# Performance work log

Measured on AMD Instinct MI355X. Metric: run time of the kernel, lower is better.

The kernel has to match this reference:

```python
import jax, jax.numpy as jnp
import numpy as np

N_NODES = 100000
N_EDGES = 1600000
N_FEATS = 64
HID1 = 128
HID2 = 128


def setup_inputs() -> dict:
    key = jax.random.key(0)
    ks = jax.random.split(key, 8)
    x = jax.random.normal(ks[0], (N_NODES, N_FEATS), dtype=jnp.float32)
    edge_index = jax.random.randint(ks[1], (2, N_EDGES), 0, N_NODES, dtype=jnp.int64)
    # glorot-ish init for linear weights (out_feats, in_feats), bias zeros (PyG default)
    W1 = jax.random.normal(ks[2], (HID1, N_FEATS), dtype=jnp.float32) * (1.0 / np.sqrt(N_FEATS))
    b1 = jnp.zeros((HID1,), dtype=jnp.float32)
    W2 = jax.random.normal(ks[3], (HID2, HID1), dtype=jnp.float32) * (1.0 / np.sqrt(HID1))
    b2 = jnp.zeros((HID2,), dtype=jnp.float32)
    W3 = jax.random.normal(ks[4], (N_FEATS, HID2), dtype=jnp.float32) * (1.0 / np.sqrt(HID2))
    b3 = jnp.zeros((N_FEATS,), dtype=jnp.float32)
    return {"x": x, "edge_index": edge_index, "W1": W1, "b1": b1,
            "W2": W2, "b2": b2, "W3": W3, "b3": b3}


def _gcn_conv(x, src, dst, norm, W, b, n_nodes):
    # dense linear transform first (out_dim may differ from in_dim)
    h = x @ W.T                                   # [N, out]
    msg = h[src] * norm[:, None]                  # gather + edge-normalize, [E+N, out]
    out = jax.ops.segment_sum(msg, dst, num_segments=n_nodes)  # scatter-add
    return out + b


def reference(x, edge_index, W1, b1, W2, b2, W3, b3):
    n = x.shape[0]
    loop = jnp.arange(n, dtype=edge_index.dtype)
    src = jnp.concatenate([edge_index[0], loop])  # self-loops appended (PyG default)
    dst = jnp.concatenate([edge_index[1], loop])
    # symmetric normalization: deg over target column incl. self-loops
    deg = jax.ops.segment_sum(jnp.ones(dst.shape, dtype=x.dtype), dst, num_segments=n)
    dinv = jnp.where(deg > 0, jax.lax.rsqrt(deg), 0.0)
    norm = dinv[src] * dinv[dst]                  # [E+N]

    h = jax.nn.relu(_gcn_conv(x, src, dst, norm, W1, b1, n))
    h = jax.nn.relu(_gcn_conv(h, src, dst, norm, W2, b2, n))
    h = _gcn_conv(h, src, dst, norm, W3, b3, n)
    return jax.nn.softmax(h, axis=1)
```

## Files before the change

kernel.cpp:

```cpp
#include <hip/hip_runtime.h>
#include <hip/hip_bf16.h>


#define NB1 256

typedef __attribute__((ext_vector_type(4))) _Float16 half4;
typedef __attribute__((ext_vector_type(8))) _Float16 half8;


__global__ __launch_bounds__(256) void k_hist(const int* __restrict__ dst, int E, int C,
                                              int NBUK, int* __restrict__ gh) {
  __shared__ int h[512];
  int t = threadIdx.x, b = blockIdx.x;
  for (int i = t; i < NBUK; i += 256) h[i] = 0;
  __syncthreads();
  int beg = b * C, end = min(beg + C, E);
  for (int i = beg + t; i < end; i += 256) atomicAdd(&h[dst[i] >> 8], 1);
  __syncthreads();
  for (int i = t; i < NBUK; i += 256) gh[i * NB1 + b] = h[i];
}

__global__ __launch_bounds__(256) void k_sum256(const int* __restrict__ g, int L,
                                                int* __restrict__ part) {
  __shared__ int red[256];
  int t = threadIdx.x;
  int idx = blockIdx.x * 256 + t;
  red[t] = (idx < L) ? g[idx] : 0;
  __syncthreads();
  for (int off = 128; off > 0; off >>= 1) {
    if (t < off) red[t] += red[t + off];
    __syncthreads();
  }
  if (t == 0) part[blockIdx.x] = red[0];
}

__global__ __launch_bounds__(512) void k_scan_part(int* __restrict__ part, int NP) {
  __shared__ int sh[512];
  int t = threadIdx.x;
  int v = (t < NP) ? part[t] : 0;
  sh[t] = v;
  __syncthreads();
  for (int off = 1; off < 512; off <<= 1) {
    int u = (t >= off) ? sh[t - off] : 0;
    __syncthreads();
    sh[t] += u;
    __syncthreads();
  }
  if (t < NP) part[t] = sh[t] - v;
}

__global__ __launch_bounds__(256) void k_scan_apply(const int* __restrict__ g, int L,
                                                    const int* __restrict__ part,
                                                    int* __restrict__ gout) {
  __shared__ int sh[256];
  int t = threadIdx.x;
  int idx = blockIdx.x * 256 + t;
  int v = (idx < L) ? g[idx] : 0;
  sh[t] = v;
  __syncthreads();
  for (int off = 1; off < 256; off <<= 1) {
    int u = (t >= off) ? sh[t - off] : 0;
    __syncthreads();
    sh[t] += u;
    __syncthreads();
  }
  if (idx < L) gout[idx] = part[blockIdx.x] + sh[t] - v;
}

__global__ __launch_bounds__(256) void k_scatter(const int* __restrict__ src,
                                                 const int* __restrict__ dst, int E, int C,
                                                 int NBUK, const int* __restrict__ gscan,
                                                 int* __restrict__ epak) {
  __shared__ int cur[512];
  int t = threadIdx.x, b = blockIdx.x;
  for (int i = t; i < NBUK; i += 256) cur[i] = gscan[i * NB1 + b];
  __syncthreads();
  int beg = b * C, end = min(beg + C, E);
  for (int i = beg + t; i < end; i += 256) {
    int d = dst[i];
    int p = atomicAdd(&cur[d >> 8], 1);
    epak[p] = src[i] | ((d & 255) << 24);
  }
}

__global__ __launch_bounds__(256) void k_csr(const int* __restrict__ epak,
                                             const int* __restrict__ gscan, int NBUK, int N, int E,
                                             int* __restrict__ rowptr, float* __restrict__ dinv,
                                             int* __restrict__ col) {
  __shared__ int cnt[256];
  __shared__ int scn[256];
  __shared__ int cur[256];
  int b = blockIdx.x, t = threadIdx.x;
  int ebeg = gscan[b * NB1];
  int eend = (b + 1 < NBUK) ? gscan[(b + 1) * NB1] : E;
  cnt[t] = 0;
  __syncthreads();
  for (int i = ebeg + t; i < eend; i += 256) atomicAdd(&cnt[(epak[i] >> 24) & 255], 1);
  __syncthreads();
  int c = cnt[t];
  scn[t] = c;
  __syncthreads();
  for (int off = 1; off < 256; off <<= 1) {
    int v = (t >= off) ? scn[t - off] : 0;
    __syncthreads();
    scn[t] += v;
    __syncthreads();
  }
  int excl = scn[t] - c;
  int node = b * 256 + t;
  if (node < N) {
    rowptr[node] = ebeg + excl;
    dinv[node] = rsqrtf((float)(c + 1));
  }
  cur[t] = ebeg + excl;
  __syncthreads();
  for (int i = ebeg + t; i < eend; i += 256) {
    int e = epak[i];
    int p = atomicAdd(&cur[(e >> 24) & 255], 1);
    col[p] = e & 0xFFFFFF;
  }
  if (b == 0 && t == 0) rowptr[N] = E;
}

__global__ __launch_bounds__(256) void k_prescaleh(const float* __restrict__ x,
                                                   const float* __restrict__ dinv,
                                                   _Float16* __restrict__ xp, int N) {
  int i = blockIdx.x * 256 + threadIdx.x;
  if (i < N * 16) {
    int row = i >> 4;
    float4 v = ((const float4*)x)[i];
    float d = dinv[row];
    half4 o;
    o[0] = (_Float16)(v.x * d);
    o[1] = (_Float16)(v.y * d);
    o[2] = (_Float16)(v.z * d);
    o[3] = (_Float16)(v.w * d);
    ((half4*)xp)[i] = o;
  }
}


template <int EPI>
__global__ __launch_bounds__(256) void k_agg64h(const _Float16* __restrict__ hp,
                                                const float* __restrict__ dinv,
                                                const int* __restrict__ rowptr,
                                                const int* __restrict__ col,
                                                const float* __restrict__ bias,
                                                float* __restrict__ out, int N) {
  int wid = blockIdx.x * 4 + (threadIdx.x >> 6);
  int lane = threadIdx.x & 63;
  if (wid >= N) return;
  int g = lane >> 3;
  int fl = (lane & 7) * 8;
  float acc[8] = {0.f, 0.f, 0.f, 0.f, 0.f, 0.f, 0.f, 0.f};
  int r0 = rowptr[wid], r1 = rowptr[wid + 1];
  for (int base = r0; base < r1; base += 64) {
    int mm = min(64, r1 - base);
    int ce = (base + lane < r1) ? col[base + lane] : 0;
    for (int j = 0; j < mm; j += 16) {
      int i0 = j + g, i1 = j + 8 + g;
      int s0 = __shfl(ce, i0);
      int s1 = __shfl(ce, i1);
      if (i0 < mm) {
        half8 v = *(const half8*)&hp[(size_t)s0 * 64 + fl];
#pragma unroll
        for (int k = 0; k < 8; ++k) acc[k] += (float)v[k];
      }
      if (i1 < mm) {
        half8 v = *(const half8*)&hp[(size_t)s1 * 64 + fl];
#pragma unroll
        for (int k = 0; k < 8; ++k) acc[k] += (float)v[k];
      }
    }
  }
#pragma unroll
  for (int o = 8; o < 64; o <<= 1) {
#pragma unroll
    for (int k = 0; k < 8; ++k) acc[k] += __shfl_xor(acc[k], o);
  }
  half8 sv = *(const half8*)&hp[(size_t)wid * 64 + fl];
  float di = dinv[wid];
  float v[8];
#pragma unroll
  for (int k = 0; k < 8; ++k) v[k] = di * (acc[k] + (float)sv[k]);
  if (EPI == 1) {
    float4 ba = *(const float4*)&bias[fl];
    float4 bb = *(const float4*)&bias[fl + 4];
    v[0] += ba.x; v[1] += ba.y; v[2] += ba.z; v[3] += ba.w;
    v[4] += bb.x; v[5] += bb.y; v[6] += bb.z; v[7] += bb.w;
    float mx = v[0];
#pragma unroll
    for (int k = 1; k < 8; ++k) mx = fmaxf(mx, v[k]);
#pragma unroll
    for (int o = 1; o < 8; o <<= 1) mx = fmaxf(mx, __shfl_xor(mx, o));
    float s = 0.f;
#pragma unroll
    for (int k = 0; k < 8; ++k) {
      v[k] = expf(v[k] - mx);
      s += v[k];
    }
#pragma unroll
    for (int o = 1; o < 8; o <<= 1) s += __shfl_xor(s, o);
    float inv = 1.0f / s;
#pragma unroll
    for (int k = 0; k < 8; ++k) v[k] *= inv;
  }
  if (lane < 8) {
    float4 o0 = make_float4(v[0], v[1], v[2], v[3]);
    float4 o1 = make_float4(v[4], v[5], v[6], v[7]);
    *(float4*)&out[(size_t)wid * 64 + fl] = o0;
    *(float4*)&out[(size_t)wid * 64 + fl + 4] = o1;
  }
}

__global__ __launch_bounds__(256) void k_agg128h(const _Float16* __restrict__ hp,
                                                 const float* __restrict__ dinv,
                                                 const int* __restrict__ rowptr,
                                                 const int* __restrict__ col,
                                                 float* __restrict__ out, int N) {
  int wid = blockIdx.x * 4 + (threadIdx.x >> 6);
  int lane = threadIdx.x & 63;
  if (wid >= N) return;
  int g = lane >> 4;
  int fl = (lane & 15) * 8;
  float acc[8] = {0.f, 0.f, 0.f, 0.f, 0.f, 0.f, 0.f, 0.f};
  int r0 = rowptr[wid], r1 = rowptr[wid + 1];
  for (int base = r0; base < r1; base += 64) {
    int mm = min(64, r1 - base);
    int ce = (base + lane < r1) ? col[base + lane] : 0;
    for (int j = 0; j < mm; j += 8) {
      int i0 = j + g, i1 = j + 4 + g;
      int s0 = __shfl(ce, i0);
      int s1 = __shfl(ce, i1);
      if (i0 < mm) {
        half8 v = *(const half8*)&hp[(size_t)s0 * 128 + fl];
#pragma unroll
        for (int k = 0; k < 8; ++k) acc[k] += (float)v[k];
      }
      if (i1 < mm) {
        half8 v = *(const half8*)&hp[(size_t)s1 * 128 + fl];
#pragma unroll
        for (int k = 0; k < 8; ++k) acc[k] += (float)v[k];
      }
    }
  }
#pragma unroll
  for (int o = 16; o < 64; o <<= 1) {
#pragma unroll
    for (int k = 0; k < 8; ++k) acc[k] += __shfl_xor(acc[k], o);
  }
  half8 sv = *(const half8*)&hp[(size_t)wid * 128 + fl];
  float di = dinv[wid];
  float v[8];
#pragma unroll
  for (int k = 0; k < 8; ++k) v[k] = di * (acc[k] + (float)sv[k]);
  if (lane < 16) {
    float4 o0 = make_float4(v[0], v[1], v[2], v[3]);
    float4 o1 = make_float4(v[4], v[5], v[6], v[7]);
    *(float4*)&out[(size_t)wid * 128 + fl] = o0;
    *(float4*)&out[(size_t)wid * 128 + fl + 4] = o1;
  }
}


template <int K, int NOUT, bool RELU, bool BIAS, bool PRESCALE, bool OUTF16>
__global__ __launch_bounds__(256) void k_gemm(const float* __restrict__ in,
                                              const float* __restrict__ W,
                                              const float* __restrict__ bias,
                                              const float* __restrict__ dinv,
                                              void* __restrict__ outp, int M) {
  constexpr int KC = 64;
  constexpr int R = 64;
  constexpr int TN = 4;
  constexpr int NG = NOUT / TN;
  constexpr int RG = 256 / NG;
  constexpr int TM = R / RG;

  __shared__ float wT[KC][NOUT + 4];
  __shared__ float inT[KC][R + 4];

  int t = threadIdx.x;
  int ng = t % NG, rg = t / NG;
  int n0 = ng * TN, r0 = rg * TM;
  int rowbase = blockIdx.x * R;

  float acc[TM][TN];
#pragma unroll
  for (int i = 0; i < TM; ++i)
#pragma unroll
    for (int j = 0; j < TN; ++j) acc[i][j] = 0.0f;

  for (int kc = 0; kc < K; kc += KC) {
    constexpr int WF4 = NOUT * KC / 4;
    for (int m = t; m < WF4; m += 256) {
      int kk4 = m % (KC / 4);
      int n = m / (KC / 4);
      const float4 w4 = *(const float4*)&W[(size_t)n * K + kc + kk4 * 4];
      wT[kk4 * 4 + 0][n] = w4.x;
      wT[kk4 * 4 + 1][n] = w4.y;
      wT[kk4 * 4 + 2][n] = w4.z;
      wT[kk4 * 4 + 3][n] = w4.w;
    }
    constexpr int IF4 = R * KC / 4;
    for (int m = t; m < IF4; m += 256) {
      int kk4 = m % (KC / 4);
      int r = m / (KC / 4);
      int row = rowbase + r;
      float4 v4 = make_float4(0.f, 0.f, 0.f, 0.f);
      if (row < M) v4 = *(const float4*)&in[(size_t)row * K + kc + kk4 * 4];
      inT[kk4 * 4 + 0][r] = v4.x;
      inT[kk4 * 4 + 1][r] = v4.y;
      inT[kk4 * 4 + 2][r] = v4.z;
      inT[kk4 * 4 + 3][r] = v4.w;
    }
    __syncthreads();

#pragma unroll 8
    for (int k = 0; k < KC; ++k) {
      float4 w4 = *(const float4*)&wT[k][n0];
      float4 iv4[TM / 4];
#pragma unroll
      for (int i4 = 0; i4 < TM / 4; ++i4) iv4[i4] = *(const float4*)&inT[k][r0 + i4 * 4];
      const float* iv = (const float*)iv4;
#pragma unroll
      for (int i = 0; i < TM; ++i) {
        acc[i][0] += iv[i] * w4.x;
        acc[i][1] += iv[i] * w4.y;
        acc[i][2] += iv[i] * w4.z;
        acc[i][3] += iv[i] * w4.w;
      }
    }
    __syncthreads();
  }

  float4 b4 = make_float4(0.f, 0.f, 0.f, 0.f);
  if (BIAS) b4 = *(const float4*)&bias[n0];
#pragma unroll
  for (int i = 0; i < TM; ++i) {
    int row = rowbase + r0 + i;
    if (row < M) {
      float4 o;
      o.x = acc[i][0] + b4.x;
      o.y = acc[i][1] + b4.y;
      o.z = acc[i][2] + b4.z;
      o.w = acc[i][3] + b4.w;
      if (RELU) {
        o.x = fmaxf(o.x, 0.f);
        o.y = fmaxf(o.y, 0.f);
        o.z = fmaxf(o.z, 0.f);
        o.w = fmaxf(o.w, 0.f);
      }
      if (PRESCALE) {
        float d = dinv[row];
        o.x *= d; o.y *= d; o.z *= d; o.w *= d;
      }
      if (OUTF16) {
        half4 h;
        h[0] = (_Float16)o.x;
        h[1] = (_Float16)o.y;
        h[2] = (_Float16)o.z;
        h[3] = (_Float16)o.w;
        *(half4*)&((_Float16*)outp)[(size_t)row * NOUT + n0] = h;
      } else {
        *(float4*)&((float*)outp)[(size_t)row * NOUT + n0] = o;
      }
    }
  }
}


extern "C" void kernel_launch(void* const* d_in, const int* in_sizes, int n_in,
                              void* d_out, int out_size, void* d_ws, size_t ws_size,
                              hipStream_t stream) {
  const float* x  = (const float*)d_in[0];
  const int*   ei = (const int*)d_in[1];
  const float* W1 = (const float*)d_in[2];
  const float* b1 = (const float*)d_in[3];
  const float* W2 = (const float*)d_in[4];
  const float* b2 = (const float*)d_in[5];
  const float* W3 = (const float*)d_in[6];
  const float* b3 = (const float*)d_in[7];
  float* out = (float*)d_out;

  const int N = in_sizes[0] / 64;
  const int E = in_sizes[1] / 2;
  const int* esrc = ei;
  const int* edst = ei + E;

  const int NBUK = (N + 255) / 256;
  const int C1 = (E + NB1 - 1) / NB1;
  const int L = NBUK * NB1;
  const int NA = (L + 255) / 256;

  char* w = (char*)d_ws;
  auto take = [&](size_t bytes) -> void* {
    void* p = (void*)w;
    w += (bytes + 255) & ~(size_t)255;
    return p;
  };
  int*   rowptr = (int*)take((size_t)(N + 1) * 4);
  float* dinv   = (float*)take((size_t)N * 4);
  int*   col    = (int*)take((size_t)E * 4);
  int*   gh     = (int*)take((size_t)L * 4);
  int*   gscan  = (int*)take((size_t)L * 4);
  int*   part   = (int*)take((size_t)NA * 4);
  _Float16* hx  = (_Float16*)take((size_t)N * 64 * 2);
  float* bufA   = (float*)take((size_t)N * 64 * 4);
  _Float16* h1  = (_Float16*)take((size_t)N * 128 * 2);
  float* bufB   = (float*)take((size_t)N * 128 * 4);
  int*   epak   = (int*)bufB;
  _Float16* hz  = hx;

  k_hist<<<NB1, 256, 0, stream>>>(edst, E, C1, NBUK, gh);
  k_sum256<<<NA, 256, 0, stream>>>(gh, L, part);
  k_scan_part<<<1, 512, 0, stream>>>(part, NA);
  k_scan_apply<<<NA, 256, 0, stream>>>(gh, L, part, gscan);
  k_scatter<<<NB1, 256, 0, stream>>>(esrc, edst, E, C1, NBUK, gscan, epak);
  k_csr<<<NBUK, 256, 0, stream>>>(epak, gscan, NBUK, N, E, rowptr, dinv, col);

  const int aggblocks = (N + 3) / 4;
  const int gemmblocks = (N + 63) / 64;

  k_prescaleh<<<(N * 16 + 255) / 256, 256, 0, stream>>>(x, dinv, hx, N);
  k_agg64h<0><<<aggblocks, 256, 0, stream>>>(hx, dinv, rowptr, col, nullptr, bufA, N);
  k_gemm<64, 128, true, true, true, true><<<gemmblocks, 256, 0, stream>>>(bufA, W1, b1, dinv, h1, N);
  k_agg128h<<<aggblocks, 256, 0, stream>>>(h1, dinv, rowptr, col, bufB, N);
  k_gemm<128, 128, true, true, false, false><<<gemmblocks, 256, 0, stream>>>(bufB, W2, b2, dinv, bufB, N);
  k_gemm<128, 64, false, false, true, true><<<gemmblocks, 256, 0, stream>>>(bufB, W3, nullptr, dinv, hz, N);
  k_agg64h<1><<<aggblocks, 256, 0, stream>>>(hz, dinv, rowptr, col, b3, out, N);
}
```

Before: 431.1 us.

## Replace FP32 SIMT GEMMs with fp16 MFMA kernels and fuse layers two and three

Swaps the shared-memory FP32 GEMM kernels for MFMA 16x16x32 fp16 kernels. A new kernel converts the weights to fp16 once per launch. The aggregation outputs are now stored as fp16 instead of fp32, which halves the intermediate traffic. The second and third linear layers are fused into one kernel that passes the intermediate through LDS. This cuts global memory traffic and ALU time but adds more fp16 rounding, and each lane reads its weight fragments directly from global memory.

```diff
diff --git a/kernel.cpp b/kernel.cpp
--- a/kernel.cpp
+++ b/kernel.cpp
@@ -6,6 +6,7 @@
 
 typedef __attribute__((ext_vector_type(4))) _Float16 half4;
 typedef __attribute__((ext_vector_type(8))) _Float16 half8;
+typedef __attribute__((ext_vector_type(4))) float f32x4;
 
 
 __global__ __launch_bounds__(256) void k_hist(const int* __restrict__ dst, int E, int C,
@@ -120,6 +121,18 @@
     col[p] = e & 0xFFFFFF;
   }
   if (b == 0 && t == 0) rowptr[N] = E;
+}
+
+__global__ __launch_bounds__(256) void k_prep_w(const float* __restrict__ W1,
+                                                const float* __restrict__ W2,
+                                                const float* __restrict__ W3,
+                                                _Float16* __restrict__ w1h,
+                                                _Float16* __restrict__ w2h,
+                                                _Float16* __restrict__ w3h) {
+  int i = blockIdx.x * 256 + threadIdx.x;
+  if (i < 128 * 64) w1h[i] = (_Float16)W1[i];
+  if (i < 128 * 128) w2h[i] = (_Float16)W2[i];
+  if (i < 64 * 128) w3h[i] = (_Float16)W3[i];
 }
 
 __global__ __launch_bounds__(256) void k_prescaleh(const float* __restrict__ x,
@@ -146,7 +159,7 @@
                                                 const int* __restrict__ rowptr,
                                                 const int* __restrict__ col,
                                                 const float* __restrict__ bias,
-                                                float* __restrict__ out, int N) {
+                                                void* __restrict__ outp, int N) {
   int wid = blockIdx.x * 4 + (threadIdx.x >> 6);
   int lane = threadIdx.x & 63;
   if (wid >= N) return;
@@ -183,7 +196,14 @@
   float v[8];
 #pragma unroll
   for (int k = 0; k < 8; ++k) v[k] = di * (acc[k] + (float)sv[k]);
-  if (EPI == 1) {
+  if (EPI == 0) {
+    if (lane < 8) {
+      half8 o;
+#pragma unroll
+      for (int k = 0; k < 8; ++k) o[k] = (_Float16)v[k];
+      *(half8*)&((_Float16*)outp)[(size_t)wid * 64 + fl] = o;
+    }
+  } else {
     float4 ba = *(const float4*)&bias[fl];
     float4 bb = *(const float4*)&bias[fl + 4];
     v[0] += ba.x; v[1] += ba.y; v[2] += ba.z; v[3] += ba.w;
@@ -204,12 +224,12 @@
     float inv = 1.0f / s;
 #pragma unroll
     for (int k = 0; k < 8; ++k) v[k] *= inv;
-  }
-  if (lane < 8) {
-    float4 o0 = make_float4(v[0], v[1], v[2], v[3]);
-    float4 o1 = make_float4(v[4], v[5], v[6], v[7]);
-    *(float4*)&out[(size_t)wid * 64 + fl] = o0;
-    *(float4*)&out[(size_t)wid * 64 + fl + 4] = o1;
+    if (lane < 8) {
+      float4 o0 = make_float4(v[0], v[1], v[2], v[3]);
+      float4 o1 = make_float4(v[4], v[5], v[6], v[7]);
+      *(float4*)&((float*)outp)[(size_t)wid * 64 + fl] = o0;
+      *(float4*)&((float*)outp)[(size_t)wid * 64 + fl + 4] = o1;
+    }
   }
 }
 
@@ -217,7 +237,7 @@
                                                  const float* __restrict__ dinv,
                                                  const int* __restrict__ rowptr,
                                                  const int* __restrict__ col,
-                                                 float* __restrict__ out, int N) {
+                                                 _Float16* __restrict__ out, int N) {
   int wid = blockIdx.x * 4 + (threadIdx.x >> 6);
   int lane = threadIdx.x & 63;
   if (wid >= N) return;
@@ -251,118 +271,154 @@
   }
   half8 sv = *(const half8*)&hp[(size_t)wid * 128 + fl];
   float di = dinv[wid];
-  float v[8];
-#pragma unroll
-  for (int k = 0; k < 8; ++k) v[k] = di * (acc[k] + (float)sv[k]);
   if (lane < 16) {
-    float4 o0 = make_float4(v[0], v[1], v[2], v[3]);
-    float4 o1 = make_float4(v[4], v[5], v[6], v[7]);
-    *(float4*)&out[(size_t)wid * 128 + fl] = o0;
-    *(float4*)&out[(size_t)wid * 128 + fl + 4] = o1;
-  }
-}
-
-
-template <int K, int NOUT, bool RELU, bool BIAS, bool PRESCALE, bool OUTF16>
-__global__ __launch_bounds__(256) void k_gemm(const float* __restrict__ in,
-                                              const float* __restrict__ W,
-                                              const float* __restrict__ bias,
-                                              const float* __restrict__ dinv,
-                                              void* __restrict__ outp, int M) {
-  constexpr int KC = 64;
-  constexpr int R = 64;
-  constexpr int TN = 4;
-  constexpr int NG = NOUT / TN;
-  constexpr int RG = 256 / NG;
-  constexpr int TM = R / RG;
-
-  __shared__ float wT[KC][NOUT + 4];
-  __shared__ float inT[KC][R + 4];
-
-  int t = threadIdx.x;
-  int ng = t % NG, rg = t / NG;
-  int n0 = ng * TN, r0 = rg * TM;
-  int rowbase = blockIdx.x * R;
-
-  float acc[TM][TN];
-#pragma unroll
-  for (int i = 0; i < TM; ++i)
-#pragma unroll
-    for (int j = 0; j < TN; ++j) acc[i][j] = 0.0f;
-
-  for (int kc = 0; kc < K; kc += KC) {
-    constexpr int WF4 = NOUT * KC / 4;
-    for (int m = t; m < WF4; m += 256) {
-      int kk4 = m % (KC / 4);
-      int n = m / (KC / 4);
-      const float4 w4 = *(const float4*)&W[(size_t)n * K + kc + kk4 * 4];
-      wT[kk4 * 4 + 0][n] = w4.x;
-      wT[kk4 * 4 + 1][n] = w4.y;
-      wT[kk4 * 4 + 2][n] = w4.z;
-      wT[kk4 * 4 + 3][n] = w4.w;
-    }
-    constexpr int IF4 = R * KC / 4;
-    for (int m = t; m < IF4; m += 256) {
-      int kk4 = m % (KC / 4);
-      int r = m / (KC / 4);
-      int row = rowbase + r;
-      float4 v4 = make_float4(0.f, 0.f, 0.f, 0.f);
-      if (row < M) v4 = *(const float4*)&in[(size_t)row * K + kc + kk4 * 4];
-      inT[kk4 * 4 + 0][r] = v4.x;
-      inT[kk4 * 4 + 1][r] = v4.y;
-      inT[kk4 * 4 + 2][r] = v4.z;
-      inT[kk4 * 4 + 3][r] = v4.w;
-    }
-    __syncthreads();
-
-#pragma unroll 8
-    for (int k = 0; k < KC; ++k) {
-      float4 w4 = *(const float4*)&wT[k][n0];
-      float4 iv4[TM / 4];
-#pragma unroll
-      for (int i4 = 0; i4 < TM / 4; ++i4) iv4[i4] = *(const float4*)&inT[k][r0 + i4 * 4];
-      const float* iv = (const float*)iv4;
-#pragma unroll
-      for (int i = 0; i < TM; ++i) {
-        acc[i][0] += iv[i] * w4.x;
-        acc[i][1] += iv[i] * w4.y;
-        acc[i][2] += iv[i] * w4.z;
-        acc[i][3] += iv[i] * w4.w;
-      }
-    }
-    __syncthreads();
-  }
-
-  float4 b4 = make_float4(0.f, 0.f, 0.f, 0.f);
-  if (BIAS) b4 = *(const float4*)&bias[n0];
-#pragma unroll
-  for (int i = 0; i < TM; ++i) {
-    int row = rowbase + r0 + i;
-    if (row < M) {
-      float4 o;
-      o.x = acc[i][0] + b4.x;
-      o.y = acc[i][1] + b4.y;
-      o.z = acc[i][2] + b4.z;
-      o.w = acc[i][3] + b4.w;
-      if (RELU) {
-        o.x = fmaxf(o.x, 0.f);
-        o.y = fmaxf(o.y, 0.f);
-        o.z = fmaxf(o.z, 0.f);
-        o.w = fmaxf(o.w, 0.f);
-      }
-      if (PRESCALE) {
-        float d = dinv[row];
-        o.x *= d; o.y *= d; o.z *= d; o.w *= d;
-      }
-      if (OUTF16) {
-        half4 h;
-        h[0] = (_Float16)o.x;
-        h[1] = (_Float16)o.y;
-        h[2] = (_Float16)o.z;
-        h[3] = (_Float16)o.w;
-        *(half4*)&((_Float16*)outp)[(size_t)row * NOUT + n0] = h;
-      } else {
-        *(float4*)&((float*)outp)[(size_t)row * NOUT + n0] = o;
+    half8 o;
+#pragma unroll
+    for (int k = 0; k < 8; ++k) o[k] = (_Float16)(di * (acc[k] + (float)sv[k]));
+    *(half8*)&out[(size_t)wid * 128 + fl] = o;
+  }
+}
+
+
+__global__ __launch_bounds__(256) void k_mfma1(const _Float16* __restrict__ a1h,
+                                               const _Float16* __restrict__ w1h,
+                                               const float* __restrict__ b1,
+                                               const float* __restrict__ dinv,
+                                               _Float16* __restrict__ h1, int N) {
+  int wave = threadIdx.x >> 6, lane = threadIdx.x & 63;
+  int rb = blockIdx.x * 128 + wave * 32;
+  if (rb >= N) return;
+  int lrow = lane & 15, lg = lane >> 4;
+
+  half8 arow[2][2];
+#pragma unroll
+  for (int rt = 0; rt < 2; ++rt) {
+    int r = rb + rt * 16 + lrow;
+    if (r >= N) r = N - 1;
+    const _Float16* p = &a1h[(size_t)r * 64 + lg * 8];
+    arow[rt][0] = *(const half8*)p;
+    arow[rt][1] = *(const half8*)(p + 32);
+  }
+  f32x4 acc[2][8];
+#pragma unroll
+  for (int rt = 0; rt < 2; ++rt)
+#pragma unroll
+    for (int nt = 0; nt < 8; ++nt) acc[rt][nt] = (f32x4){0.f, 0.f, 0.f, 0.f};
+
+#pragma unroll
+  for (int nt = 0; nt < 8; ++nt) {
+#pragma unroll
+    for (int ks = 0; ks < 2; ++ks) {
+      half8 wf = *(const half8*)&w1h[(size_t)(nt * 16 + lrow) * 64 + ks * 32 + lg * 8];
+      acc[0][nt] = __builtin_amdgcn_mfma_f32_16x16x32_f16(wf, arow[0][ks], acc[0][nt], 0, 0, 0);
+      acc[1][nt] = __builtin_amdgcn_mfma_f32_16x16x32_f16(wf, arow[1][ks], acc[1][nt], 0, 0, 0);
+    }
+  }
+#pragma unroll
+  for (int rt = 0; rt < 2; ++rt) {
+    int r = rb + rt * 16 + lrow;
+    if (r < N) {
+      float di = dinv[r];
+#pragma unroll
+      for (int nt = 0; nt < 8; ++nt) {
+        int n = nt * 16 + lg * 4;
+        float4 bb = *(const float4*)&b1[n];
+        half4 o;
+        o[0] = (_Float16)(fmaxf(acc[rt][nt][0] + bb.x, 0.f) * di);
+        o[1] = (_Float16)(fmaxf(acc[rt][nt][1] + bb.y, 0.f) * di);
+        o[2] = (_Float16)(fmaxf(acc[rt][nt][2] + bb.z, 0.f) * di);
+        o[3] = (_Float16)(fmaxf(acc[rt][nt][3] + bb.w, 0.f) * di);
+        *(half4*)&h1[(size_t)r * 128 + n] = o;
+      }
+    }
+  }
+}
+
+__global__ __launch_bounds__(256) void k_mfma23(const _Float16* __restrict__ a2h,
+                                                const _Float16* __restrict__ w2h,
+                                                const float* __restrict__ b2,
+                                                const _Float16* __restrict__ w3h,
+                                                const float* __restrict__ dinv,
+                                                _Float16* __restrict__ hz, int N) {
+  __shared__ _Float16 u_lds[4][32][136];
+  int wave = threadIdx.x >> 6, lane = threadIdx.x & 63;
+  int rb = blockIdx.x * 128 + wave * 32;
+  if (rb >= N) return;
+  int lrow = lane & 15, lg = lane >> 4;
+
+  half8 frag[2][4];
+#pragma unroll
+  for (int rt = 0; rt < 2; ++rt) {
+    int r = rb + rt * 16 + lrow;
+    if (r >= N) r = N - 1;
+    const _Float16* p = &a2h[(size_t)r * 128 + lg * 8];
+#pragma unroll
+    for (int ks = 0; ks < 4; ++ks) frag[rt][ks] = *(const half8*)(p + ks * 32);
+  }
+  f32x4 acc[2][8];
+#pragma unroll
+  for (int rt = 0; rt < 2; ++rt)
+#pragma unroll
+    for (int nt = 0; nt < 8; ++nt) acc[rt][nt] = (f32x4){0.f, 0.f, 0.f, 0.f};
+
+#pragma unroll
+  for (int nt = 0; nt < 8; ++nt) {
+#pragma unroll
+    for (int ks = 0; ks < 4; ++ks) {
+      half8 wf = *(const half8*)&w2h[(size_t)(nt * 16 + lrow) * 128 + ks * 32 + lg * 8];
+      acc[0][nt] = __builtin_amdgcn_mfma_f32_16x16x32_f16(wf, frag[0][ks], acc[0][nt], 0, 0, 0);
+      acc[1][nt] = __builtin_amdgcn_mfma_f32_16x16x32_f16(wf, frag[1][ks], acc[1][nt], 0, 0, 0);
+    }
+  }
+#pragma unroll
+  for (int rt = 0; rt < 2; ++rt) {
+#pragma unroll
+    for (int nt = 0; nt < 8; ++nt) {
+      int n = nt * 16 + lg * 4;
+      float4 bb = *(const float4*)&b2[n];
+      half4 o;
+      o[0] = (_Float16)fmaxf(acc[rt][nt][0] + bb.x, 0.f);
+      o[1] = (_Float16)fmaxf(acc[rt][nt][1] + bb.y, 0.f);
+      o[2] = (_Float16)fmaxf(acc[rt][nt][2] + bb.z, 0.f);
+      o[3] = (_Float16)fmaxf(acc[rt][nt][3] + bb.w, 0.f);
+      *(half4*)&u_lds[wave][rt * 16 + lrow][n] = o;
+    }
+  }
+#pragma unroll
+  for (int rt = 0; rt < 2; ++rt)
+#pragma unroll
+    for (int ks = 0; ks < 4; ++ks)
+      frag[rt][ks] = *(const half8*)&u_lds[wave][rt * 16 + lrow][ks * 32 + lg * 8];
+
+  f32x4 acc2[2][4];
+#pragma unroll
+  for (int rt = 0; rt < 2; ++rt)
+#pragma unroll
+    for (int mt = 0; mt < 4; ++mt) acc2[rt][mt] = (f32x4){0.f, 0.f, 0.f, 0.f};
+
+#pragma unroll
+  for (int mt = 0; mt < 4; ++mt) {
+#pragma unroll
+    for (int ks = 0; ks < 4; ++ks) {
+      half8 wf = *(const half8*)&w3h[(size_t)(mt * 16 + lrow) * 128 + ks * 32 + lg * 8];
+      acc2[0][mt] = __builtin_amdgcn_mfma_f32_16x16x32_f16(wf, frag[0][ks], acc2[0][mt], 0, 0, 0);
+      acc2[1][mt] = __builtin_amdgcn_mfma_f32_16x16x32_f16(wf, frag[1][ks], acc2[1][mt], 0, 0, 0);
+    }
+  }
+#pragma unroll
+  for (int rt = 0; rt < 2; ++rt) {
+    int r = rb + rt * 16 + lrow;
+    if (r < N) {
+      float di = dinv[r];
+#pragma unroll
+      for (int mt = 0; mt < 4; ++mt) {
+        int m = mt * 16 + lg * 4;
+        half4 o;
+        o[0] = (_Float16)(acc2[rt][mt][0] * di);
+        o[1] = (_Float16)(acc2[rt][mt][1] * di);
+        o[2] = (_Float16)(acc2[rt][mt][2] * di);
+        o[3] = (_Float16)(acc2[rt][mt][3] * di);
+        *(half4*)&hz[(size_t)r * 64 + m] = o;
       }
     }
   }
@@ -404,11 +460,14 @@
   int*   gh     = (int*)take((size_t)L * 4);
   int*   gscan  = (int*)take((size_t)L * 4);
   int*   part   = (int*)take((size_t)NA * 4);
+  _Float16* w1h = (_Float16*)take((size_t)128 * 64 * 2);
+  _Float16* w2h = (_Float16*)take((size_t)128 * 128 * 2);
+  _Float16* w3h = (_Float16*)take((size_t)64 * 128 * 2);
   _Float16* hx  = (_Float16*)take((size_t)N * 64 * 2);
-  float* bufA   = (float*)take((size_t)N * 64 * 4);
+  _Float16* a1h = (_Float16*)take((size_t)N * 64 * 2);
   _Float16* h1  = (_Float16*)take((size_t)N * 128 * 2);
-  float* bufB   = (float*)take((size_t)N * 128 * 4);
-  int*   epak   = (int*)bufB;
+  _Float16* a2h = (_Float16*)take((size_t)N * 128 * 2);
+  int*   epak   = (int*)h1;
   _Float16* hz  = hx;
 
   k_hist<<<NB1, 256, 0, stream>>>(edst, E, C1, NBUK, gh);
@@ -418,14 +477,15 @@
   k_scatter<<<NB1, 256, 0, stream>>>(esrc, edst, E, C1, NBUK, gscan, epak);
   k_csr<<<NBUK, 256, 0, stream>>>(epak, gscan, NBUK, N, E, rowptr, dinv, col);
 
+  k_prep_w<<<64, 256, 0, stream>>>(W1, W2, W3, w1h, w2h, w3h);
+
   const int aggblocks = (N + 3) / 4;
-  const int gemmblocks = (N + 63) / 64;
+  const int mfmablocks = (N + 127) / 128;
 
   k_prescaleh<<<(N * 16 + 255) / 256, 256, 0, stream>>>(x, dinv, hx, N);
-  k_agg64h<0><<<aggblocks, 256, 0, stream>>>(hx, dinv, rowptr, col, nullptr, bufA, N);
-  k_gemm<64, 128, true, true, true, true><<<gemmblocks, 256, 0, stream>>>(bufA, W1, b1, dinv, h1, N);
-  k_agg128h<<<aggblocks, 256, 0, stream>>>(h1, dinv, rowptr, col, bufB, N);
-  k_gemm<128, 128, true, true, false, false><<<gemmblocks, 256, 0, stream>>>(bufB, W2, b2, dinv, bufB, N);
-  k_gemm<128, 64, false, false, true, true><<<gemmblocks, 256, 0, stream>>>(bufB, W3, nullptr, dinv, hz, N);
+  k_agg64h<0><<<aggblocks, 256, 0, stream>>>(hx, dinv, rowptr, col, nullptr, a1h, N);
+  k_mfma1<<<mfmablocks, 256, 0, stream>>>(a1h, w1h, b1, dinv, h1, N);
+  k_agg128h<<<aggblocks, 256, 0, stream>>>(h1, dinv, rowptr, col, a2h, N);
+  k_mfma23<<<mfmablocks, 256, 0, stream>>>(a2h, w2h, b2, w3h, dinv, hz, N);
   k_agg64h<1><<<aggblocks, 256, 0, stream>>>(hz, dinv, rowptr, col, b3, out, N);
 }
```

Result: faster. 357.6 us (-17.0%).
